# Kernel optimization log

Hardware: AMD Instinct MI355X
Metric: run time of the kernel (lower is better)

Reference implementation:

```python
import jax, jax.numpy as jnp
import numpy as np

N = 100000
E = 1600000
F = 64
H = 64
C = 10


def setup_inputs() -> dict:
    key = jax.random.key(0)
    ks = jax.random.split(key, 8)
    x = jax.random.normal(ks[0], (N, F), dtype=jnp.float32)
    edge_index = jax.random.randint(ks[1], (2, E), 0, N, dtype=jnp.int64)
    s = 1.0 / np.sqrt(H)
    enc_w = jax.random.uniform(ks[2], (F, H), jnp.float32, -s, s)
    enc_b = jax.random.uniform(ks[3], (H,), jnp.float32, -s, s)
    proc_w = jax.random.uniform(ks[4], (H, H), jnp.float32, -s, s)
    proc_b = jax.random.uniform(ks[5], (H,), jnp.float32, -s, s)
    dec_w = jax.random.uniform(ks[6], (H, C), jnp.float32, -s, s)
    dec_b = jax.random.uniform(ks[7], (C,), jnp.float32, -s, s)
    return {"x": x, "edge_index": edge_index, "diameter": 6,
            "enc_w": enc_w, "enc_b": enc_b,
            "proc_w": proc_w, "proc_b": proc_b,
            "dec_w": dec_w, "dec_b": dec_b}


def reference(x, edge_index, diameter, enc_w, enc_b, proc_w, proc_b, dec_w, dec_b):
    # encoder
    h = x @ enc_w + enc_b  # [N, H]
    src = edge_index[0]
    dst = edge_index[1]
    n = x.shape[0]
    # GINConv (eps=0, aggr='max'): h = nn(h + scatter_max_j h_j)
    for _ in range(diameter):
        agg = jax.ops.segment_max(h[src], dst, num_segments=n)  # [N, H]
        agg = jnp.where(jnp.isfinite(agg), agg, 0.0)  # empty segments -> 0
        h = (h + agg) @ proc_w + proc_b
    # single decoder head, node-level log-softmax
    return jax.nn.log_softmax(h @ dec_w + dec_b, axis=-1)
```

## Files before the change

### kernel.cpp

```cpp
#include <hip/hip_runtime.h>
#include <hip/hip_fp16.h>
#include <math.h>


#define NPW 8
#define NPG 16
#define CAP 64
#define CSTRIDE 16

typedef unsigned short ushort_t;
typedef unsigned int uint_t;
typedef _Float16 half8 __attribute__((ext_vector_type(8)));
typedef float floatx4 __attribute__((ext_vector_type(4)));
typedef uint_t uintx4 __attribute__((ext_vector_type(4)));
typedef int intx4 __attribute__((ext_vector_type(4)));

__device__ __forceinline__ uint_t pkmax(uint_t a, uint_t b) {
    uint_t r;
    asm volatile("v_pk_max_f16 %0, %1, %2" : "=v"(r) : "v"(a), "v"(b));
    return r;
}
__device__ __forceinline__ uintx4 pkmax4(uintx4 a, uintx4 b) {
    uintx4 r;
    r.x = pkmax(a.x, b.x);
    r.y = pkmax(a.y, b.y);
    r.z = pkmax(a.z, b.z);
    r.w = pkmax(a.w, b.w);
    return r;
}
__device__ __forceinline__ uintx4 shmax4(uintx4 m, int msk) {
    uintx4 t;
    t.x = (uint_t)__shfl_xor((int)m.x, msk);
    t.y = (uint_t)__shfl_xor((int)m.y, msk);
    t.z = (uint_t)__shfl_xor((int)m.z, msk);
    t.w = (uint_t)__shfl_xor((int)m.w, msk);
    return pkmax4(m, t);
}
__device__ __forceinline__ ushort_t f2h(float x) {
    return __half_as_ushort(__float2half_rn(x));
}
__device__ __forceinline__ float h2f_lo(uint_t u) {
    return __half2float(__ushort_as_half((ushort_t)(u & 0xFFFF)));
}
__device__ __forceinline__ float h2f_hi(uint_t u) {
    return __half2float(__ushort_as_half((ushort_t)(u >> 16)));
}
__device__ __forceinline__ int uclamp(int i, int n) {
    uint_t u = (uint_t)i, un = (uint_t)n;
    return (int)(u < un ? u : un);
}

__global__ void zero_i32(int* __restrict__ p, int n) {
    int i = blockIdx.x * blockDim.x + threadIdx.x;
    if (i < n) p[i] = 0;
}

__global__ void fill_sentinel_h(ushort_t* __restrict__ ha, ushort_t* __restrict__ hb, int n) {
    int lane = threadIdx.x;
    if (lane < 64) {
        ha[(size_t)n * 64 + lane] = 0xFC00;
        hb[(size_t)n * 64 + lane] = 0xFC00;
    }
}

__global__ void pad_fill(const int* __restrict__ cur, int* __restrict__ csr, int n) {
    int node = blockIdx.x * blockDim.x + threadIdx.x;
    if (node < n) {
        int d = cur[(size_t)node * CSTRIDE];
        d = (d > CAP) ? CAP : d;
        int end = (d + 7) & ~7;
        end = (end > CAP) ? CAP : end;
        for (int s = d; s < end; s++) csr[(size_t)node * CAP + s] = n;
    }
}

__global__ __launch_bounds__(256) void scatter_xcd(const int* __restrict__ src,
                                                   const int* __restrict__ dst,
                                                   int E, int n,
                                                   int* __restrict__ cursor,
                                                   int* __restrict__ csr_src) {
    int part = blockIdx.x & 7;
    int bip = blockIdx.x >> 3;
    int nGroups = gridDim.x >> 3;
    int lo = (int)(((long long)part * n) >> 3);
    int hi = (int)(((long long)(part + 1) * n) >> 3);
    int stride = nGroups * blockDim.x;
    int E4 = E >> 2;
    const intx4* dst4 = (const intx4*)dst;
    for (int i = bip * blockDim.x + threadIdx.x; i < E4; i += stride) {
        intx4 d4 = __builtin_nontemporal_load(&dst4[i]);
        if (d4.x >= lo && d4.x < hi) {
            int s = __builtin_nontemporal_load(&src[4 * i + 0]);
            int pos = atomicAdd(&cursor[(size_t)d4.x * CSTRIDE], 1);
            if (pos < CAP) csr_src[(size_t)d4.x * CAP + pos] = s;
        }
        if (d4.y >= lo && d4.y < hi) {
            int s = __builtin_nontemporal_load(&src[4 * i + 1]);
            int pos = atomicAdd(&cursor[(size_t)d4.y * CSTRIDE], 1);
            if (pos < CAP) csr_src[(size_t)d4.y * CAP + pos] = s;
        }
        if (d4.z >= lo && d4.z < hi) {
            int s = __builtin_nontemporal_load(&src[4 * i + 2]);
            int pos = atomicAdd(&cursor[(size_t)d4.z * CSTRIDE], 1);
            if (pos < CAP) csr_src[(size_t)d4.z * CAP + pos] = s;
        }
        if (d4.w >= lo && d4.w < hi) {
            int s = __builtin_nontemporal_load(&src[4 * i + 3]);
            int pos = atomicAdd(&cursor[(size_t)d4.w * CSTRIDE], 1);
            if (pos < CAP) csr_src[(size_t)d4.w * CAP + pos] = s;
        }
    }
    if (bip == 0 && threadIdx.x < (E & 3)) {
        int i = (E & ~3) + threadIdx.x;
        int d = dst[i];
        if (d >= lo && d < hi) {
            int s = src[i];
            int pos = atomicAdd(&cursor[(size_t)d * CSTRIDE], 1);
            if (pos < CAP) csr_src[(size_t)d * CAP + pos] = s;
        }
    }
}

__device__ __forceinline__ void gemm8(const float* __restrict__ Ws,
                                      const float (*hsw)[64],
                                      float bias, int lane, float acc[NPW]) {
#pragma unroll
    for (int r = 0; r < NPW; r++) acc[r] = bias;
#pragma unroll 1
    for (int kc = 0; kc < 8; kc++) {
        float wreg[8];
#pragma unroll
        for (int j = 0; j < 8; j++) wreg[j] = Ws[(kc * 8 + j) * 64 + lane];
#pragma unroll
        for (int r = 0; r < NPW; r++) {
            float4 a = *(const float4*)&hsw[r][kc * 8];
            float4 c = *(const float4*)&hsw[r][kc * 8 + 4];
            acc[r] = fmaf(a.x, wreg[0], acc[r]);
            acc[r] = fmaf(a.y, wreg[1], acc[r]);
            acc[r] = fmaf(a.z, wreg[2], acc[r]);
            acc[r] = fmaf(a.w, wreg[3], acc[r]);
            acc[r] = fmaf(c.x, wreg[4], acc[r]);
            acc[r] = fmaf(c.y, wreg[5], acc[r]);
            acc[r] = fmaf(c.z, wreg[6], acc[r]);
            acc[r] = fmaf(c.w, wreg[7], acc[r]);
        }
    }
}

__global__ __launch_bounds__(256, 4) void encode_k(const float* __restrict__ x,
                                                   const float* __restrict__ w,
                                                   const float* __restrict__ b,
                                                   ushort_t* __restrict__ h2, int n) {
    __shared__ float Ws[64 * 64];
    __shared__ float hs[4][NPW][64];
    {
        const float4* w4 = (const float4*)w;
        float4* s4 = (float4*)Ws;
        for (int i = threadIdx.x; i < 1024; i += 256) s4[i] = w4[i];
    }
    int wv = threadIdx.x >> 6;
    int lane = threadIdx.x & 63;
    int base = (blockIdx.x * 4 + wv) * NPW;

#pragma unroll
    for (int r = 0; r < NPW; r++) {
        int node = base + r;
        if (node < n) hs[wv][r][lane] = x[(size_t)node * 64 + lane];
    }
    __syncthreads();

    float bias = b[lane];
    float acc[NPW];
    gemm8(Ws, hs[wv], bias, lane, acc);

#pragma unroll
    for (int r = 0; r < NPW; r++) {
        int node = base + r;
        if (node < n) h2[(size_t)node * 64 + lane] = f2h(acc[r]);
    }
}

__global__ __launch_bounds__(256, 6) void gin16_k(const ushort_t* __restrict__ h2in,
                                                  ushort_t* __restrict__ h2out,
                                                  const int* __restrict__ degcur,
                                                  const int* __restrict__ csr_src,
                                                  const float* __restrict__ w,
                                                  const float* __restrict__ bias,
                                                  int n) {
    __shared__ __align__(16) ushort_t Wt[64 * 72];
    __shared__ __align__(16) ushort_t hs2[4][NPG * 72];

    for (int i = threadIdx.x; i < 4096; i += 256) {
        int k = i >> 6, nn = i & 63;
        Wt[nn * 72 + k] = f2h(w[i]);
    }
    __syncthreads();

    int wv = threadIdx.x >> 6, lane = threadIdx.x & 63;
    int f8 = lane & 7;
    int sub3 = lane >> 3;
    int base = (blockIdx.x * 4 + wv) * NPG;
    const uintx4* hq = (const uintx4*)h2in;
    ushort_t* myhs = hs2[wv];

#pragma unroll 2
    for (int rp = 0; rp < NPG; rp++) {
        int node = base + rp;
        bool v = node < n;
        int d = v ? degcur[(size_t)node * CSTRIDE] : 0;
        d = (d > CAP) ? CAP : d;
        const int4* ip = (const int4*)&csr_src[(size_t)(v ? node : 0) * CAP];
        int4 i0 = ip[sub3];
        uintx4 a0 = hq[(size_t)uclamp(i0.x, n) * 8 + f8];
        uintx4 a1 = hq[(size_t)uclamp(i0.y, n) * 8 + f8];
        uintx4 a2 = hq[(size_t)uclamp(i0.z, n) * 8 + f8];
        uintx4 a3 = hq[(size_t)uclamp(i0.w, n) * 8 + f8];
        uintx4 m = pkmax4(pkmax4(a0, a1), pkmax4(a2, a3));
        if (d > 32) {
            int4 i1 = ip[8 + sub3];
            uintx4 c0 = hq[(size_t)uclamp(i1.x, n) * 8 + f8];
            uintx4 c1 = hq[(size_t)uclamp(i1.y, n) * 8 + f8];
            uintx4 c2 = hq[(size_t)uclamp(i1.z, n) * 8 + f8];
            uintx4 c3 = hq[(size_t)uclamp(i1.w, n) * 8 + f8];
            m = pkmax4(m, pkmax4(pkmax4(c0, c1), pkmax4(c2, c3)));
        }
        m = shmax4(m, 8);
        m = shmax4(m, 16);
        m = shmax4(m, 32);
        if (sub3 == 0 && v) {
            uintx4 s = hq[(size_t)node * 8 + f8];
            float r0 = h2f_lo(s.x), r1 = h2f_hi(s.x);
            float r2 = h2f_lo(s.y), r3 = h2f_hi(s.y);
            float r4 = h2f_lo(s.z), r5 = h2f_hi(s.z);
            float r6 = h2f_lo(s.w), r7 = h2f_hi(s.w);
            if (d > 0) {
                r0 += h2f_lo(m.x); r1 += h2f_hi(m.x);
                r2 += h2f_lo(m.y); r3 += h2f_hi(m.y);
                r4 += h2f_lo(m.z); r5 += h2f_hi(m.z);
                r6 += h2f_lo(m.w); r7 += h2f_hi(m.w);
            }
            uintx4 o;
            o.x = (uint_t)f2h(r0) | ((uint_t)f2h(r1) << 16);
            o.y = (uint_t)f2h(r2) | ((uint_t)f2h(r3) << 16);
            o.z = (uint_t)f2h(r4) | ((uint_t)f2h(r5) << 16);
            o.w = (uint_t)f2h(r6) | ((uint_t)f2h(r7) << 16);
            *(uintx4*)&myhs[rp * 72 + f8 * 8] = o;
        }
    }

    int m = lane & 15, quad = lane >> 4;
    float b0 = bias[m], b1 = bias[16 + m], b2 = bias[32 + m], b3 = bias[48 + m];
    floatx4 c0 = {0.f, 0.f, 0.f, 0.f}, c1 = c0, c2 = c0, c3 = c0;
#pragma unroll
    for (int kt = 0; kt < 2; kt++) {
        half8 a = *(const half8*)&myhs[m * 72 + kt * 32 + quad * 8];
        half8 w0 = *(const half8*)&Wt[(m) * 72 + kt * 32 + quad * 8];
        half8 w1 = *(const half8*)&Wt[(16 + m) * 72 + kt * 32 + quad * 8];
        half8 w2 = *(const half8*)&Wt[(32 + m) * 72 + kt * 32 + quad * 8];
        half8 w3 = *(const half8*)&Wt[(48 + m) * 72 + kt * 32 + quad * 8];
        c0 = __builtin_amdgcn_mfma_f32_16x16x32_f16(a, w0, c0, 0, 0, 0);
        c1 = __builtin_amdgcn_mfma_f32_16x16x32_f16(a, w1, c1, 0, 0, 0);
        c2 = __builtin_amdgcn_mfma_f32_16x16x32_f16(a, w2, c2, 0, 0, 0);
        c3 = __builtin_amdgcn_mfma_f32_16x16x32_f16(a, w3, c3, 0, 0, 0);
    }
#pragma unroll
    for (int i = 0; i < 4; i++) {
        int row = quad * 4 + i;
        myhs[row * 72 + m]      = f2h(c0[i] + b0);
        myhs[row * 72 + 16 + m] = f2h(c1[i] + b1);
        myhs[row * 72 + 32 + m] = f2h(c2[i] + b2);
        myhs[row * 72 + 48 + m] = f2h(c3[i] + b3);
    }
#pragma unroll
    for (int r = 0; r < NPG; r++) {
        int node = base + r;
        if (node < n) h2out[(size_t)node * 64 + lane] = myhs[r * 72 + lane];
    }
}

__global__ __launch_bounds__(256) void decode_k(const ushort_t* __restrict__ h,
                                                const float* __restrict__ w,
                                                const float* __restrict__ b,
                                                float* __restrict__ out, int n) {
    int wv = threadIdx.x >> 6;
    int lane = threadIdx.x & 63;
    int node = blockIdx.x * 4 + wv;
    if (node >= n) return;
    float hv = __half2float(__ushort_as_half(h[(size_t)node * 64 + lane]));
    float l[10];
#pragma unroll
    for (int c = 0; c < 10; c++) l[c] = hv * w[lane * 10 + c];
#pragma unroll
    for (int off = 32; off >= 1; off >>= 1) {
#pragma unroll
        for (int c = 0; c < 10; c++) l[c] += __shfl_down(l[c], off);
    }
    if (lane == 0) {
        float mx = -INFINITY;
#pragma unroll
        for (int c = 0; c < 10; c++) { l[c] += b[c]; mx = fmaxf(mx, l[c]); }
        float sum = 0.0f;
#pragma unroll
        for (int c = 0; c < 10; c++) sum += expf(l[c] - mx);
        float lse = mx + logf(sum);
#pragma unroll
        for (int c = 0; c < 10; c++) out[(size_t)node * 10 + c] = l[c] - lse;
    }
}

extern "C" void kernel_launch(void* const* d_in, const int* in_sizes, int n_in,
                              void* d_out, int out_size, void* d_ws, size_t ws_size,
                              hipStream_t stream) {
    const float* x     = (const float*)d_in[0];
    const int*   ei    = (const int*)d_in[1];
    const float* enc_w = (const float*)d_in[3];
    const float* enc_b = (const float*)d_in[4];
    const float* proc_w = (const float*)d_in[5];
    const float* proc_b = (const float*)d_in[6];
    const float* dec_w = (const float*)d_in[7];
    const float* dec_b = (const float*)d_in[8];
    float* out = (float*)d_out;

    const int n = in_sizes[0] / 64;
    const int E = in_sizes[1] / 2;
    const int* src = ei;
    const int* dst = ei + E;

    char* p = (char*)d_ws;
    ushort_t* h_a = (ushort_t*)p;    p += (size_t)(n + 1) * 64 * sizeof(ushort_t);
    ushort_t* h_b = (ushort_t*)p;    p += (size_t)(n + 1) * 64 * sizeof(ushort_t);
    int* cur = (int*)p;              p += (size_t)n * CSTRIDE * sizeof(int);
    int* csr = (int*)p;              p += (size_t)n * CAP * sizeof(int);

    const int gN = (n + 255) / 256;
    const int gC = (n * CSTRIDE + 255) / 256;
    const int gTileE = (n + 4 * NPW - 1) / (4 * NPW);
    const int gTileG = (n + 4 * NPG - 1) / (4 * NPG);
    const int gNode = (n + 3) / 4;

    zero_i32<<<gC, 256, 0, stream>>>(cur, n * CSTRIDE);
    fill_sentinel_h<<<1, 64, 0, stream>>>(h_a, h_b, n);
    scatter_xcd<<<2048, 256, 0, stream>>>(src, dst, E, n, cur, csr);
    pad_fill<<<gN, 256, 0, stream>>>(cur, csr, n);

    encode_k<<<gTileE, 256, 0, stream>>>(x, enc_w, enc_b, h_a, n);

    ushort_t* hi = h_a;
    ushort_t* ho = h_b;
    for (int it = 0; it < 6; it++) {
        gin16_k<<<gTileG, 256, 0, stream>>>(hi, ho, cur, csr, proc_w, proc_b, n);
        ushort_t* t = hi; hi = ho; ho = t;
    }

    decode_k<<<gNode, 256, 0, stream>>>(hi, dec_w, dec_b, out, n);
}
```

Baseline: 488.4 us.

## Fuse edge scatter with encoder launch, compact cursor array, drop pad kernel

Measured after the change: 485.1 us. No clear change (-0.7%).

```diff
diff --git a/kernel.cpp b/kernel.cpp
--- a/kernel.cpp
+++ b/kernel.cpp
@@ -6,7 +6,7 @@
 #define NPW 8
 #define NPG 16
 #define CAP 64
-#define CSTRIDE 16
+#define SCB 2048
 
 typedef unsigned short ushort_t;
 typedef unsigned int uint_t;
@@ -50,74 +50,13 @@
     return (int)(u < un ? u : un);
 }
 
-__global__ void zero_i32(int* __restrict__ p, int n) {
+__global__ void prep_k(int* __restrict__ cur, int n,
+                       ushort_t* __restrict__ ha, ushort_t* __restrict__ hb) {
     int i = blockIdx.x * blockDim.x + threadIdx.x;
-    if (i < n) p[i] = 0;
-}
-
-__global__ void fill_sentinel_h(ushort_t* __restrict__ ha, ushort_t* __restrict__ hb, int n) {
-    int lane = threadIdx.x;
-    if (lane < 64) {
-        ha[(size_t)n * 64 + lane] = 0xFC00;
-        hb[(size_t)n * 64 + lane] = 0xFC00;
-    }
-}
-
-__global__ void pad_fill(const int* __restrict__ cur, int* __restrict__ csr, int n) {
-    int node = blockIdx.x * blockDim.x + threadIdx.x;
-    if (node < n) {
-        int d = cur[(size_t)node * CSTRIDE];
-        d = (d > CAP) ? CAP : d;
-        int end = (d + 7) & ~7;
-        end = (end > CAP) ? CAP : end;
-        for (int s = d; s < end; s++) csr[(size_t)node * CAP + s] = n;
-    }
-}
-
-__global__ __launch_bounds__(256) void scatter_xcd(const int* __restrict__ src,
-                                                   const int* __restrict__ dst,
-                                                   int E, int n,
-                                                   int* __restrict__ cursor,
-                                                   int* __restrict__ csr_src) {
-    int part = blockIdx.x & 7;
-    int bip = blockIdx.x >> 3;
-    int nGroups = gridDim.x >> 3;
-    int lo = (int)(((long long)part * n) >> 3);
-    int hi = (int)(((long long)(part + 1) * n) >> 3);
-    int stride = nGroups * blockDim.x;
-    int E4 = E >> 2;
-    const intx4* dst4 = (const intx4*)dst;
-    for (int i = bip * blockDim.x + threadIdx.x; i < E4; i += stride) {
-        intx4 d4 = __builtin_nontemporal_load(&dst4[i]);
-        if (d4.x >= lo && d4.x < hi) {
-            int s = __builtin_nontemporal_load(&src[4 * i + 0]);
-            int pos = atomicAdd(&cursor[(size_t)d4.x * CSTRIDE], 1);
-            if (pos < CAP) csr_src[(size_t)d4.x * CAP + pos] = s;
-        }
-        if (d4.y >= lo && d4.y < hi) {
-            int s = __builtin_nontemporal_load(&src[4 * i + 1]);
-            int pos = atomicAdd(&cursor[(size_t)d4.y * CSTRIDE], 1);
-            if (pos < CAP) csr_src[(size_t)d4.y * CAP + pos] = s;
-        }
-        if (d4.z >= lo && d4.z < hi) {
-            int s = __builtin_nontemporal_load(&src[4 * i + 2]);
-            int pos = atomicAdd(&cursor[(size_t)d4.z * CSTRIDE], 1);
-            if (pos < CAP) csr_src[(size_t)d4.z * CAP + pos] = s;
-        }
-        if (d4.w >= lo && d4.w < hi) {
-            int s = __builtin_nontemporal_load(&src[4 * i + 3]);
-            int pos = atomicAdd(&cursor[(size_t)d4.w * CSTRIDE], 1);
-            if (pos < CAP) csr_src[(size_t)d4.w * CAP + pos] = s;
-        }
-    }
-    if (bip == 0 && threadIdx.x < (E & 3)) {
-        int i = (E & ~3) + threadIdx.x;
-        int d = dst[i];
-        if (d >= lo && d < hi) {
-            int s = src[i];
-            int pos = atomicAdd(&cursor[(size_t)d * CSTRIDE], 1);
-            if (pos < CAP) csr_src[(size_t)d * CAP + pos] = s;
-        }
+    if (i < n) cur[i] = 0;
+    if (blockIdx.x == 0 && threadIdx.x < 64) {
+        ha[(size_t)n * 64 + threadIdx.x] = 0xFC00;
+        hb[(size_t)n * 64 + threadIdx.x] = 0xFC00;
     }
 }
 
@@ -147,36 +86,82 @@
     }
 }
 
-__global__ __launch_bounds__(256, 4) void encode_k(const float* __restrict__ x,
-                                                   const float* __restrict__ w,
-                                                   const float* __restrict__ b,
-                                                   ushort_t* __restrict__ h2, int n) {
-    __shared__ float Ws[64 * 64];
-    __shared__ float hs[4][NPW][64];
-    {
-        const float4* w4 = (const float4*)w;
-        float4* s4 = (float4*)Ws;
-        for (int i = threadIdx.x; i < 1024; i += 256) s4[i] = w4[i];
-    }
-    int wv = threadIdx.x >> 6;
-    int lane = threadIdx.x & 63;
-    int base = (blockIdx.x * 4 + wv) * NPW;
-
-#pragma unroll
-    for (int r = 0; r < NPW; r++) {
-        int node = base + r;
-        if (node < n) hs[wv][r][lane] = x[(size_t)node * 64 + lane];
-    }
-    __syncthreads();
-
-    float bias = b[lane];
-    float acc[NPW];
-    gemm8(Ws, hs[wv], bias, lane, acc);
-
-#pragma unroll
-    for (int r = 0; r < NPW; r++) {
-        int node = base + r;
-        if (node < n) h2[(size_t)node * 64 + lane] = f2h(acc[r]);
+__global__ __launch_bounds__(256, 4) void scatter_encode_k(
+        const int* __restrict__ src, const int* __restrict__ dst,
+        int E, int n,
+        int* __restrict__ cursor, int* __restrict__ csr_src,
+        const float* __restrict__ x, const float* __restrict__ w,
+        const float* __restrict__ b, ushort_t* __restrict__ h2) {
+    if (blockIdx.x < SCB) {
+        int part = blockIdx.x & 7;
+        int bip = blockIdx.x >> 3;
+        int nGroups = SCB >> 3;
+        int lo = (int)(((long long)part * n) >> 3);
+        int hi = (int)(((long long)(part + 1) * n) >> 3);
+        int stride = nGroups * blockDim.x;
+        int E4 = E >> 2;
+        const intx4* dst4 = (const intx4*)dst;
+        for (int i = bip * blockDim.x + threadIdx.x; i < E4; i += stride) {
+            intx4 d4 = __builtin_nontemporal_load(&dst4[i]);
+            if (d4.x >= lo && d4.x < hi) {
+                int s = __builtin_nontemporal_load(&src[4 * i + 0]);
+                int pos = atomicAdd(&cursor[d4.x], 1);
+                if (pos < CAP) csr_src[(size_t)d4.x * CAP + pos] = s;
+            }
+            if (d4.y >= lo && d4.y < hi) {
+                int s = __builtin_nontemporal_load(&src[4 * i + 1]);
+                int pos = atomicAdd(&cursor[d4.y], 1);
+                if (pos < CAP) csr_src[(size_t)d4.y * CAP + pos] = s;
+            }
+            if (d4.z >= lo && d4.z < hi) {
+                int s = __builtin_nontemporal_load(&src[4 * i + 2]);
+                int pos = atomicAdd(&cursor[d4.z], 1);
+                if (pos < CAP) csr_src[(size_t)d4.z * CAP + pos] = s;
+            }
+            if (d4.w >= lo && d4.w < hi) {
+                int s = __builtin_nontemporal_load(&src[4 * i + 3]);
+                int pos = atomicAdd(&cursor[d4.w], 1);
+                if (pos < CAP) csr_src[(size_t)d4.w * CAP + pos] = s;
+            }
+        }
+        if (bip == 0 && threadIdx.x < (E & 3)) {
+            int i = (E & ~3) + threadIdx.x;
+            int d = dst[i];
+            if (d >= lo && d < hi) {
+                int s = src[i];
+                int pos = atomicAdd(&cursor[d], 1);
+                if (pos < CAP) csr_src[(size_t)d * CAP + pos] = s;
+            }
+        }
+    } else {
+        __shared__ float Ws[64 * 64];
+        __shared__ float hs[4][NPW][64];
+        int eb = blockIdx.x - SCB;
+        {
+            const float4* w4 = (const float4*)w;
+            float4* s4 = (float4*)Ws;
+            for (int i = threadIdx.x; i < 1024; i += 256) s4[i] = w4[i];
+        }
+        int wv = threadIdx.x >> 6;
+        int lane = threadIdx.x & 63;
+        int base = (eb * 4 + wv) * NPW;
+
+#pragma unroll
+        for (int r = 0; r < NPW; r++) {
+            int node = base + r;
+            if (node < n) hs[wv][r][lane] = x[(size_t)node * 64 + lane];
+        }
+        __syncthreads();
+
+        float bias = b[lane];
+        float acc[NPW];
+        gemm8(Ws, hs[wv], bias, lane, acc);
+
+#pragma unroll
+        for (int r = 0; r < NPW; r++) {
+            int node = base + r;
+            if (node < n) h2[(size_t)node * 64 + lane] = f2h(acc[r]);
+        }
     }
 }
 
@@ -207,7 +192,7 @@
     for (int rp = 0; rp < NPG; rp++) {
         int node = base + rp;
         bool v = node < n;
-        int d = v ? degcur[(size_t)node * CSTRIDE] : 0;
+        int d = v ? degcur[node] : 0;
         d = (d > CAP) ? CAP : d;
         const int4* ip = (const int4*)&csr_src[(size_t)(v ? node : 0) * CAP];
         int4 i0 = ip[sub3];
@@ -329,21 +314,17 @@
     char* p = (char*)d_ws;
     ushort_t* h_a = (ushort_t*)p;    p += (size_t)(n + 1) * 64 * sizeof(ushort_t);
     ushort_t* h_b = (ushort_t*)p;    p += (size_t)(n + 1) * 64 * sizeof(ushort_t);
-    int* cur = (int*)p;              p += (size_t)n * CSTRIDE * sizeof(int);
+    int* cur = (int*)p;              p += (size_t)n * sizeof(int);
     int* csr = (int*)p;              p += (size_t)n * CAP * sizeof(int);
 
     const int gN = (n + 255) / 256;
-    const int gC = (n * CSTRIDE + 255) / 256;
     const int gTileE = (n + 4 * NPW - 1) / (4 * NPW);
     const int gTileG = (n + 4 * NPG - 1) / (4 * NPG);
     const int gNode = (n + 3) / 4;
 
-    zero_i32<<<gC, 256, 0, stream>>>(cur, n * CSTRIDE);
-    fill_sentinel_h<<<1, 64, 0, stream>>>(h_a, h_b, n);
-    scatter_xcd<<<2048, 256, 0, stream>>>(src, dst, E, n, cur, csr);
-    pad_fill<<<gN, 256, 0, stream>>>(cur, csr, n);
-
-    encode_k<<<gTileE, 256, 0, stream>>>(x, enc_w, enc_b, h_a, n);
+    prep_k<<<gN, 256, 0, stream>>>(cur, n, h_a, h_b);
+    scatter_encode_k<<<SCB + gTileE, 256, 0, stream>>>(src, dst, E, n, cur, csr,
+                                                       x, enc_w, enc_b, h_a);
 
     ushort_t* hi = h_a;
     ushort_t* ho = h_b;
```
